# Performance work log

Hardware: AMD Instinct MI355X
Metric: run time of the kernel (lower is better)

Reference implementation:

```python
import jax, jax.numpy as jnp
import numpy as np
from jax import lax

DN = ('NCHW', 'OIHW', 'NCHW')


def conv3x3(x, w, groups=1):
    return lax.conv_general_dilated(x, w, window_strides=(1, 1),
                                    padding=((1, 1), (1, 1)),
                                    dimension_numbers=DN,
                                    feature_group_count=groups)


def conv1x1(x, w):
    return lax.conv_general_dilated(x, w, window_strides=(1, 1),
                                    padding=((0, 0), (0, 0)),
                                    dimension_numbers=DN)


def l2_normalize(t, eps=1e-12):
    n = jnp.sqrt(jnp.sum(t * t, axis=-1, keepdims=True))
    return t / jnp.maximum(n, eps)


def setup_inputs() -> dict:
    key = jax.random.key(0)
    ks = jax.random.split(key, 10)
    B, C, H, W = 4, 64, 256, 256
    heads = 8
    s = 0.05
    return {
        'x': jax.random.normal(ks[0], (B, C, H, W), jnp.float32),
        'w_iem': jax.random.normal(ks[1], (C, C, 3, 3), jnp.float32) * s,
        'w_nem': jax.random.normal(ks[2], (C, C, 3, 3), jnp.float32) * s,
        'w_iem_dw': jax.random.normal(ks[3], (C, 1, 3, 3), jnp.float32) * s,
        'w_nem_dw': jax.random.normal(ks[4], (C, 1, 3, 3), jnp.float32) * s,
        'w_q': jax.random.normal(ks[5], (C, C, 1, 1), jnp.float32) * s,
        'w_k': jax.random.normal(ks[6], (C, C, 1, 1), jnp.float32) * s,
        'w_v': jax.random.normal(ks[7], (C, C, 1, 1), jnp.float32) * s,
        'w_proj': jax.random.normal(ks[8], (C, C, 1, 1), jnp.float32) * s,
        'temperature': jnp.ones((1, heads, 1, 1, 1, 1), jnp.float32),
    }


def igam_forward(x, w_iem, w_nem, w_iem_dw, w_nem_dw, w_q, w_k, w_v, w_proj,
                 temperature, num_heads=8, window_size=8):
    b, c, h, w = x.shape
    ws = window_size
    pad_h = (ws - h % ws) % ws
    pad_w = (ws - w % ws) % ws
    if pad_h or pad_w:  # replicate pad on right/bottom (static)
        x = jnp.pad(x, ((0, 0), (0, 0), (0, pad_h), (0, pad_w)), mode='edge')
    hp, wp = x.shape[-2:]
    heads = num_heads
    d = c // heads
    nh, nw = hp // ws, wp // ws

    illumination_map = conv3x3(jax.nn.sigmoid(conv3x3(x, w_iem)), w_iem_dw, groups=c)
    noise_map = conv3x3(jax.nn.sigmoid(conv3x3(x, w_nem)), w_nem_dw, groups=c)
    illum_scalar = jnp.mean(illumination_map, axis=1, keepdims=True)  # (b,1,hp,wp)
    noise_scalar = jnp.mean(noise_map, axis=1, keepdims=True)

    q = conv1x1(illumination_map, w_q)
    k = conv1x1(noise_map, w_k)
    v = conv1x1(x, w_v)

    def to_windows(t):  # (b,c,hp,wp) -> (b,heads,nh,nw,ws*ws,d)
        t = t.reshape(b, heads, d, hp, wp).transpose(0, 1, 3, 4, 2)
        t = t.reshape(b, heads, nh, ws, nw, ws, d).transpose(0, 1, 2, 4, 3, 5, 6)
        return t.reshape(b, heads, nh, nw, ws * ws, d)

    def scalar_to_windows(t):  # (b,1,hp,wp) -> (b,1,nh,nw,ws*ws,1)
        t = t.reshape(b, 1, nh, ws, nw, ws).transpose(0, 1, 2, 4, 3, 5)
        return t.reshape(b, 1, nh, nw, ws * ws, 1)

    qw = l2_normalize(to_windows(q)) * (1.0 + scalar_to_windows(illum_scalar))
    kw = l2_normalize(to_windows(k)) * jnp.clip(1.0 - scalar_to_windows(noise_scalar), 0.0, 1.0)
    vw = to_windows(v)

    scale = d ** (-0.5)
    attn = jnp.einsum('bhnmqd,bhnmkd->bhnmqk', qw, kw) * scale * temperature
    attn = jax.nn.softmax(attn, axis=-1)
    outw = jnp.einsum('bhnmqk,bhnmkd->bhnmqd', attn, vw)

    # merge windows back to (b, c, hp, wp)
    outw = outw.reshape(b, heads, nh, nw, ws, ws, d).transpose(0, 1, 6, 2, 4, 3, 5)
    out = outw.reshape(b, heads * d, nh * ws, nw * ws)
    if pad_h or pad_w:
        out = out[:, :, :h, :w]
    return conv1x1(out, w_proj)


def reference(x, w_iem, w_nem, w_iem_dw, w_nem_dw, w_q, w_k, w_v, w_proj,
              temperature):
    return igam_forward(x, w_iem, w_nem, w_iem_dw, w_nem_dw, w_q, w_k, w_v,
                        w_proj, temperature)
```

## Files before the change

### kernel.cpp

```cpp
#include <hip/hip_runtime.h>
#include <math.h>

#define W_ 256
#define H_ 256
#define HW 65536
#define CC 64

typedef _Float16 h16;
typedef _Float16 half8 __attribute__((ext_vector_type(8)));
typedef float f32x4  __attribute__((ext_vector_type(4)));
typedef float f32x16 __attribute__((ext_vector_type(16)));

__device__ __forceinline__ unsigned pk2(float a, float b) {
  union { h16 h[2]; unsigned u; } c;
  c.h[0] = (h16)a; c.h[1] = (h16)b;
  return c.u;
}
__device__ __forceinline__ void plswap(unsigned &a, unsigned &b) {
  asm volatile("v_permlane32_swap_b32 %0, %1" : "+v"(a), "+v"(b));
}

__global__ __launch_bounds__(256) void k_wprep(
    const float* __restrict__ wi, const float* __restrict__ wn, h16* __restrict__ Bt)
{
  int i = blockIdx.x * 256 + threadIdx.x;
  if (i >= 128 * 576) return;
  int co = i / 576, k = i - co * 576;
  int tap = k >> 6, ci = k & 63;
  const float* src = (co < 64) ? wi : wn;
  int c = co & 63;
  Bt[i] = (h16)src[(c * 64 + ci) * 9 + tap];
}

__global__ __launch_bounds__(256) void k_wprep2(
    const float* __restrict__ wq, const float* __restrict__ wk,
    const float* __restrict__ wv, const float* __restrict__ wp,
    const float* __restrict__ wdw1, const float* __restrict__ wdw2,
    h16* __restrict__ W)
{
  int i = blockIdx.x * 256 + threadIdx.x;
  if (i >= 17536) return;
  if (i < 16384) {
    int m = i >> 12, e = i & 4095;
    const float* s = (m == 0) ? wq : (m == 1) ? wk : (m == 2) ? wv : wp;
    W[i] = (h16)s[e];
  } else {
    int e = i - 16384;
    int pass = e / 576, rem = e - pass * 576;
    int tap = rem >> 6, c = rem & 63;
    const float* s = pass ? wdw2 : wdw1;
    W[i] = (h16)s[c * 9 + tap];
  }
}

__global__ __launch_bounds__(256) void k_xpose(
    const float* __restrict__ x, h16* __restrict__ xT)
{
  __shared__ __align__(16) char sm[64 * 132];
  const int tid = threadIdx.x;
  const int xt = blockIdx.x, y = blockIdx.y, b = blockIdx.z;
  const int x0 = xt * 64;
  const float* xb = x + ((size_t)b * CC) * HW + y * W_ + x0;
  const int ci = tid >> 2, q = tid & 3;
#pragma unroll
  for (int k = 0; k < 4; ++k) {
    const int pc = q + k * 4;
    float4 v = *(const float4*)(xb + (size_t)ci * HW + pc * 4);
    const int px = pc * 4;
    *(h16*)(sm + (px + 0) * 132 + ci * 2) = (h16)v.x;
    *(h16*)(sm + (px + 1) * 132 + ci * 2) = (h16)v.y;
    *(h16*)(sm + (px + 2) * 132 + ci * 2) = (h16)v.z;
    *(h16*)(sm + (px + 3) * 132 + ci * 2) = (h16)v.w;
  }
  __syncthreads();
  h16* dst = xT + (((size_t)b * 256 + y) * 256 + x0) * 64;
#pragma unroll
  for (int it = 0; it < 2; ++it) {
    int task = tid + it * 256;
    int px = task >> 3, c8 = task & 7;
    int4 d = *(const int4*)(sm + px * 132 + c8 * 16);
    *(int4*)(dst + px * 64 + c8 * 8) = d;
  }
}

__global__ __launch_bounds__(512) void k_conv3x3x2(
    const h16* __restrict__ xT, const h16* __restrict__ Bt,
    h16* __restrict__ T1, h16* __restrict__ T2)
{
  __shared__ __align__(16) char lds[38016];

  const int tid = threadIdx.x;
  const int b = blockIdx.z, ry = blockIdx.y, cx = blockIdx.x;
  const int y0 = ry * 2, x0 = cx * 64;

  {
    const h16* xb = xT + ((size_t)b * 256) * 256 * 64;
    int4 zero4; zero4.x = zero4.y = zero4.z = zero4.w = 0;
#pragma unroll
    for (int it = 0; it < 5; ++it) {
      int idx = tid + it * 512;
      if (idx < 2112) {
        int pxr = idx >> 3, c8 = idx & 7;
        int r = pxr / 66, c = pxr - r * 66;
        int gy = y0 - 1 + r, gx = x0 - 1 + c;
        int4 d = zero4;
        if ((unsigned)gy < 256u && (unsigned)gx < 256u)
          d = *(const int4*)(xb + ((size_t)(gy * 256 + gx)) * 64 + c8 * 8);
        *(int4*)(lds + pxr * 144 + c8 * 16) = d;
      }
    }
  }
  __syncthreads();

  const int wv = tid >> 6, lane = tid & 63;
  const int wn_ = wv & 3;
  const int wm_ = wv >> 2;
  const int cob = wn_ * 32;
  const int pxb = wm_ * 64;
  const int lg = lane >> 4, lr = lane & 15;

  const char* pB[4];
#pragma unroll
  for (int pi = 0; pi < 4; ++pi) {
    int opx = (pxb + pi * 16 + lr) & 63;
    pB[pi] = lds + (wm_ * 66 + opx) * 144 + lg * 16;
  }
  const h16* wb0 = Bt + (size_t)(cob + lr) * 576 + lg * 8;
  const h16* wb1 = wb0 + 16 * 576;

  f32x4 acc[2][4];
#pragma unroll
  for (int i = 0; i < 2; ++i)
#pragma unroll
    for (int j = 0; j < 4; ++j) acc[i][j] = (f32x4){0.f, 0.f, 0.f, 0.f};

#pragma unroll
  for (int tap = 0; tap < 9; ++tap) {
    const int dy = tap / 3, dx = tap - dy * 3;
#pragma unroll
    for (int kh = 0; kh < 2; ++kh) {
      const int loff = (dy * 66 + dx) * 144 + kh * 64;
      const int koff = tap * 64 + kh * 32;
      half8 a0 = *(const half8*)(wb0 + koff);
      half8 a1 = *(const half8*)(wb1 + koff);
      half8 b0 = *(const half8*)(pB[0] + loff);
      half8 b1 = *(const half8*)(pB[1] + loff);
      half8 b2 = *(const half8*)(pB[2] + loff);
      half8 b3 = *(const half8*)(pB[3] + loff);
      acc[0][0] = __builtin_amdgcn_mfma_f32_16x16x32_f16(a0, b0, acc[0][0], 0, 0, 0);
      acc[0][1] = __builtin_amdgcn_mfma_f32_16x16x32_f16(a0, b1, acc[0][1], 0, 0, 0);
      acc[0][2] = __builtin_amdgcn_mfma_f32_16x16x32_f16(a0, b2, acc[0][2], 0, 0, 0);
      acc[0][3] = __builtin_amdgcn_mfma_f32_16x16x32_f16(a0, b3, acc[0][3], 0, 0, 0);
      acc[1][0] = __builtin_amdgcn_mfma_f32_16x16x32_f16(a1, b0, acc[1][0], 0, 0, 0);
      acc[1][1] = __builtin_amdgcn_mfma_f32_16x16x32_f16(a1, b1, acc[1][1], 0, 0, 0);
      acc[1][2] = __builtin_amdgcn_mfma_f32_16x16x32_f16(a1, b2, acc[1][2], 0, 0, 0);
      acc[1][3] = __builtin_amdgcn_mfma_f32_16x16x32_f16(a1, b3, acc[1][3], 0, 0, 0);
    }
  }
  __syncthreads();

#pragma unroll
  for (int ni = 0; ni < 2; ++ni) {
#pragma unroll
    for (int pi = 0; pi < 4; ++pi) {
      const int opx = (pxb + pi * 16 + lr) & 63;
      const int pxid = wm_ * 64 + opx;
      const int co = cob + ni * 16 + lg * 4;
      float s0 = 1.f / (1.f + __expf(-acc[ni][pi][0]));
      float s1 = 1.f / (1.f + __expf(-acc[ni][pi][1]));
      float s2 = 1.f / (1.f + __expf(-acc[ni][pi][2]));
      float s3 = 1.f / (1.f + __expf(-acc[ni][pi][3]));
      uint2 d; d.x = pk2(s0, s1); d.y = pk2(s2, s3);
      *(uint2*)(lds + pxid * 272 + co * 2) = d;
    }
  }
  __syncthreads();

  {
    int px = tid >> 3, chg = tid & 7;
#pragma unroll
    for (int seg = 0; seg < 4; ++seg) {
      int t = seg >> 1, rr = seg & 1;
      int4 d = *(const int4*)(lds + (rr * 64 + px) * 272 + t * 128 + chg * 16);
      h16* dst = (t ? T2 : T1) + (((size_t)b * 256 + (y0 + rr)) * 256 + (x0 + px)) * 64 + chg * 8;
      *(int4*)dst = d;
    }
  }
}

#define HALO 0
#define DWW  14400
#define SIN  16704
#define INA  17216
#define INB  26432
#define INC  35648

__global__ __launch_bounds__(256, 3) void k_megaattn(
    const h16* __restrict__ T1g, const h16* __restrict__ T2g,
    const h16* __restrict__ xT, const h16* __restrict__ Wall,
    const float* __restrict__ temp, float* __restrict__ out)
{
  __shared__ __align__(16) char sm[44864];
  const int tid = threadIdx.x;
  const int wv = tid >> 6, lane = tid & 63;
  const int lg = lane >> 4, lr = lane & 15;

  const int u = blockIdx.x;
  const int xcd = u & 7, idx = u >> 3;
  const int flat = xcd * 512 + idx;
  const int b = flat >> 10, rem = flat & 1023;
  const int wy = rem >> 5, wx = rem & 31;
  const int y0 = wy * 8, x0 = wx * 8;

  half8 wf[4][2];
#pragma unroll
  for (int m = 0; m < 4; ++m)
#pragma unroll
    for (int ks = 0; ks < 2; ++ks)
      wf[m][ks] = *(const half8*)(Wall + m * 4096 + (wv * 16 + lr) * 64 + ks * 32 + lg * 8);
  const float t0 = temp[wv * 2], t1 = temp[wv * 2 + 1];

  int4 zero4; zero4.x = zero4.y = zero4.z = zero4.w = 0;
  int4 h1r[4], h2r[4], xtr[2];
#pragma unroll
  for (int i = 0; i < 4; ++i) {
    int cc = tid + i * 256;
    bool act = cc < 800;
    int prow = act ? (cc >> 3) : 0;
    int c8 = cc & 7;
    int hy = prow / 10, hx = prow - hy * 10;
    int gy = y0 - 1 + hy, gx = x0 - 1 + hx;
    bool ok = act && (unsigned)gy < 256u && (unsigned)gx < 256u;
    size_t ga = (((size_t)b * 256 + gy) * 256 + gx) * (size_t)64 + c8 * 8;
    h1r[i] = ok ? *(const int4*)(T1g + ga) : zero4;
    h2r[i] = ok ? *(const int4*)(T2g + ga) : zero4;
  }
  const size_t wbase = (((size_t)b * 256 + y0) * 256 + x0) * 64;
#pragma unroll
  for (int it = 0; it < 2; ++it) {
    int p = tid + it * 256;
    int py = p >> 6, off = p & 63;
    xtr[it] = *(const int4*)(xT + wbase + (size_t)py * 16384 + off * 8);
  }

#pragma unroll
  for (int i = 0; i < 4; ++i) {
    int cc = tid + i * 256;
    if (cc < 800) *(int4*)(sm + HALO + (cc >> 3) * 144 + (cc & 7) * 16) = h1r[i];
  }
#pragma unroll
  for (int it = 0; it < 2; ++it) {
    int p = tid + it * 256;
    int py = p >> 6, off = p & 63;
    int px = py * 8 + (off >> 3);
    *(int4*)(sm + INC + px * 144 + (off & 7) * 16) = xtr[it];
  }
  if (tid < 144) {
    int4 d = *(const int4*)(Wall + 16384 + tid * 8);
    *(int4*)(sm + DWW + tid * 16) = d;
  }
  __syncthreads();

#pragma unroll
  for (int pass = 0; pass < 2; ++pass) {
    const int outb = pass ? INB : INA;
#pragma unroll
    for (int it = 0; it < 2; ++it) {
      const int task = it * 256 + tid;
      const int px = task >> 3, c8 = task & 7;
      const int py = px >> 3, pxx = px & 7;
      float a[8];
#pragma unroll
      for (int j = 0; j < 8; ++j) a[j] = 0.f;
#pragma unroll
      for (int tap = 0; tap < 9; ++tap) {
        const int dy = tap / 3, dx = tap - dy * 3;
        half8 v  = *(const half8*)(sm + HALO + ((py + dy) * 10 + pxx + dx) * 144 + c8 * 16);
        half8 w8 = *(const half8*)(sm + DWW + pass * 1152 + tap * 128 + c8 * 16);
#pragma unroll
        for (int j = 0; j < 8; ++j) a[j] = fmaf((float)v[j], (float)w8[j], a[j]);
      }
      half8 o;
#pragma unroll
      for (int j = 0; j < 8; ++j) o[j] = (h16)a[j];
      *(half8*)(sm + outb + px * 144 + c8 * 16) = o;
    }
    __syncthreads();
    if (pass == 0) {
#pragma unroll
      for (int i = 0; i < 4; ++i) {
        int cc = tid + i * 256;
        if (cc < 800) *(int4*)(sm + HALO + (cc >> 3) * 144 + (cc & 7) * 16) = h2r[i];
      }
      __syncthreads();
    }
  }

  if (tid < 128) {
    int which = tid >> 6, px = tid & 63;
    const char* row = sm + (which ? INB : INA) + px * 144;
    float s = 0.f;
#pragma unroll
    for (int j = 0; j < 8; ++j) {
      half8 v = *(const half8*)(row + j * 16);
#pragma unroll
      for (int e = 0; e < 8; ++e) s += (float)v[e];
    }
    *(float*)(sm + SIN + which * 256 + px * 4) = s * (1.f / 64.f);
  }
  __syncthreads();

  f32x4 aq[4], ak[4], av[4];
#pragma unroll
  for (int pi = 0; pi < 4; ++pi) {
    aq[pi] = (f32x4){0.f, 0.f, 0.f, 0.f};
    ak[pi] = (f32x4){0.f, 0.f, 0.f, 0.f};
    av[pi] = (f32x4){0.f, 0.f, 0.f, 0.f};
  }
#pragma unroll
  for (int pi = 0; pi < 4; ++pi)
#pragma unroll
    for (int ks = 0; ks < 2; ++ks) {
      const int boff = (pi * 16 + lr) * 144 + ks * 64 + lg * 16;
      half8 b0 = *(const half8*)(sm + INA + boff);
      half8 b1 = *(const half8*)(sm + INB + boff);
      half8 b2 = *(const half8*)(sm + INC + boff);
      aq[pi] = __builtin_amdgcn_mfma_f32_16x16x32_f16(wf[0][ks], b0, aq[pi], 0, 0, 0);
      ak[pi] = __builtin_amdgcn_mfma_f32_16x16x32_f16(wf[1][ks], b1, ak[pi], 0, 0, 0);
      av[pi] = __builtin_amdgcn_mfma_f32_16x16x32_f16(wf[2][ks], b2, av[pi], 0, 0, 0);
    }
  __syncthreads();

  const float th = (lg & 2) ? t1 : t0;
#pragma unroll
  for (int pi = 0; pi < 4; ++pi) {
    const int px = pi * 16 + lr;
    const float si = *(const float*)(sm + SIN + px * 4);
    const float sn = *(const float*)(sm + SIN + 256 + px * 4);
    float s2 = aq[pi][0]*aq[pi][0] + aq[pi][1]*aq[pi][1] + aq[pi][2]*aq[pi][2] + aq[pi][3]*aq[pi][3];
    float qs = (1.f + si) * 0.35355339059327373f * th /
               fmaxf(sqrtf(s2 + __shfl_xor(s2, 16)), 1e-12f);
    float k2 = ak[pi][0]*ak[pi][0] + ak[pi][1]*ak[pi][1] + ak[pi][2]*ak[pi][2] + ak[pi][3]*ak[pi][3];
    float ks2 = fminf(fmaxf(1.f - sn, 0.f), 1.f) /
                fmaxf(sqrtf(k2 + __shfl_xor(k2, 16)), 1e-12f);
    uint2 dq; dq.x = pk2(aq[pi][0]*qs, aq[pi][1]*qs); dq.y = pk2(aq[pi][2]*qs, aq[pi][3]*qs);
    uint2 dk; dk.x = pk2(ak[pi][0]*ks2, ak[pi][1]*ks2); dk.y = pk2(ak[pi][2]*ks2, ak[pi][3]*ks2);
    *(uint2*)(sm + INA + px * 144 + (wv * 16 + lg * 4) * 2) = dq;
    *(uint2*)(sm + INB + px * 144 + (wv * 16 + lg * 4) * 2) = dk;
#pragma unroll
    for (int r = 0; r < 4; ++r)
      *(h16*)(sm + INC + (wv * 16 + lg * 4 + r) * 144 + px * 2) = (h16)av[pi][r];
  }
  __syncthreads();

  const int l31 = lane & 31, hi = lane >> 5;
  const half8 hz = {(h16)0, (h16)0, (h16)0, (h16)0, (h16)0, (h16)0, (h16)0, (h16)0};
  const f32x16 z16 = {0.f,0.f,0.f,0.f,0.f,0.f,0.f,0.f,0.f,0.f,0.f,0.f,0.f,0.f,0.f,0.f};

#pragma unroll
  for (int t = 0; t < 2; ++t) {
    const int h = wv * 2 + t;
    half8 kfr[2], qfr[2];
#pragma unroll
    for (int kt = 0; kt < 2; ++kt)
      kfr[kt] = hi ? hz : *(const half8*)(sm + INB + (kt * 32 + l31) * 144 + h * 16);
#pragma unroll
    for (int qt = 0; qt < 2; ++qt)
      qfr[qt] = hi ? hz : *(const half8*)(sm + INA + (qt * 32 + l31) * 144 + h * 16);

#pragma unroll
    for (int qt = 0; qt < 2; ++qt) {
      f32x16 s0 = __builtin_amdgcn_mfma_f32_32x32x16_f16(kfr[0], qfr[qt], z16, 0, 0, 0);
      f32x16 s1 = __builtin_amdgcn_mfma_f32_32x32x16_f16(kfr[1], qfr[qt], z16, 0, 0, 0);
      float mx = s0[0];
#pragma unroll
      for (int i = 1; i < 16; ++i) mx = fmaxf(mx, s0[i]);
#pragma unroll
      for (int i = 0; i < 16; ++i) mx = fmaxf(mx, s1[i]);
      mx = fmaxf(mx, __shfl_xor(mx, 32));
      float sum = 0.f;
#pragma unroll
      for (int i = 0; i < 16; ++i) { s0[i] = __expf(s0[i] - mx); sum += s0[i]; }
#pragma unroll
      for (int i = 0; i < 16; ++i) { s1[i] = __expf(s1[i] - mx); sum += s1[i]; }
      sum += __shfl_xor(sum, 32);
      const float inv = 1.f / sum;
#pragma unroll
      for (int i = 0; i < 16; ++i) { s0[i] *= inv; s1[i] *= inv; }

      half8 pa[4];
#pragma unroll
      for (int st = 0; st < 4; ++st) {
        const int rb = (st & 1) * 8;
        float p0, p1, p2, p3, p4, p5, p6, p7;
        if (st < 2) {
          p0 = s0[rb+0]; p1 = s0[rb+1]; p2 = s0[rb+2]; p3 = s0[rb+3];
          p4 = s0[rb+4]; p5 = s0[rb+5]; p6 = s0[rb+6]; p7 = s0[rb+7];
        } else {
          p0 = s1[rb+0]; p1 = s1[rb+1]; p2 = s1[rb+2]; p3 = s1[rb+3];
          p4 = s1[rb+4]; p5 = s1[rb+5]; p6 = s1[rb+6]; p7 = s1[rb+7];
        }
        unsigned x0_ = pk2(p0, p1), x1_ = pk2(p2, p3);
        unsigned y0_ = pk2(p4, p5), y1_ = pk2(p6, p7);
        plswap(x0_, y0_);
        plswap(x1_, y1_);
        union { unsigned uu4[4]; half8 h; } uu;
        uu.uu4[0] = x0_; uu.uu4[1] = x1_; uu.uu4[2] = y0_; uu.uu4[3] = y1_;
        pa[st] = uu.h;
      }
      f32x16 oacc = z16;
#pragma unroll
      for (int st = 0; st < 4; ++st) {
        half8 vfr = (l31 < 8)
          ? *(const half8*)(sm + INC + (h * 8 + l31) * 144 + (st * 16 + hi * 8) * 2)
          : hz;
        oacc = __builtin_amdgcn_mfma_f32_32x32x16_f16(pa[st], vfr, oacc, 0, 0, 0);
      }
      if (l31 < 8) {
#pragma unroll
        for (int r = 0; r < 16; ++r) {
          const int q = qt * 32 + (r & 3) + 8 * (r >> 2) + 4 * hi;
          *(h16*)(sm + INA + q * 144 + (h * 8 + l31) * 2) = (h16)oacc[r];
        }
      }
    }
  }
  __syncthreads();

  f32x4 pacc[4];
#pragma unroll
  for (int pi = 0; pi < 4; ++pi) pacc[pi] = (f32x4){0.f, 0.f, 0.f, 0.f};
#pragma unroll
  for (int pi = 0; pi < 4; ++pi)
#pragma unroll
    for (int ks = 0; ks < 2; ++ks) {
      half8 bfr = *(const half8*)(sm + INA + (pi * 16 + lr) * 144 + ks * 64 + lg * 16);
      pacc[pi] = __builtin_amdgcn_mfma_f32_16x16x32_f16(wf[3][ks], bfr, pacc[pi], 0, 0, 0);
    }
#pragma unroll
  for (int pi = 0; pi < 4; ++pi) {
    const int px = pi * 16 + lr;
    const int py = px >> 3, pxx = px & 7;
    const int co = wv * 16 + lg * 4;
    float* ob = out + ((size_t)(b * CC + co)) * HW + (size_t)(y0 + py) * W_ + (x0 + pxx);
    ob[0]      = pacc[pi][0];
    ob[HW]     = pacc[pi][1];
    ob[2 * HW] = pacc[pi][2];
    ob[3 * HW] = pacc[pi][3];
  }
}

extern "C" void kernel_launch(void* const* d_in, const int* in_sizes, int n_in,
                              void* d_out, int out_size, void* d_ws, size_t ws_size,
                              hipStream_t stream) {
  const float* x        = (const float*)d_in[0];
  const float* w_iem    = (const float*)d_in[1];
  const float* w_nem    = (const float*)d_in[2];
  const float* w_iem_dw = (const float*)d_in[3];
  const float* w_nem_dw = (const float*)d_in[4];
  const float* w_q      = (const float*)d_in[5];
  const float* w_k      = (const float*)d_in[6];
  const float* w_v      = (const float*)d_in[7];
  const float* w_proj   = (const float*)d_in[8];
  const float* temp     = (const float*)d_in[9];
  float* outp = (float*)d_out;

  const size_t PLE = (size_t)4 * CC * HW;
  h16* h0   = (h16*)d_ws;
  h16* T1   = h0;
  h16* T2   = h0 + PLE;
  h16* xT   = h0 + 2 * PLE;
  h16* Bt   = h0 + 3 * PLE;
  h16* Wall = Bt + 73728;

  dim3 b256(256), b512(512);

  k_wprep    <<<dim3(288),        b256, 0, stream>>>(w_iem, w_nem, Bt);
  k_wprep2   <<<dim3(69),         b256, 0, stream>>>(w_q, w_k, w_v, w_proj,
                                                     w_iem_dw, w_nem_dw, Wall);
  k_xpose    <<<dim3(4, 256, 4),  b256, 0, stream>>>(x, xT);
  k_conv3x3x2<<<dim3(4, 128, 4),  b512, 0, stream>>>(xT, Bt, T1, T2);
  k_megaattn <<<dim3(4096),       b256, 0, stream>>>(T1, T2, xT, Wall, temp, outp);
}
```

Baseline: 228.0 us.

## Double megaattn block to 512 threads and compute depthwise conv in packed fp16

Launches the fused attention kernel with 512 threads per window instead of 256. Each wave now handles one head and half the pixels of the 1x1 projections, so per-thread loop trip counts halve and latency hiding can improve. The depthwise 3x3 now accumulates in fp16 packed vectors instead of fp32 FMAs, which cuts ALU work but loses accumulation precision. The launch-bounds request of 6 blocks of 512 threads per CU may squeeze registers and force spills.

```diff
diff --git a/kernel.cpp b/kernel.cpp
--- a/kernel.cpp
+++ b/kernel.cpp
@@ -195,7 +195,7 @@
 #define INB  26432
 #define INC  35648
 
-__global__ __launch_bounds__(256, 3) void k_megaattn(
+__global__ __launch_bounds__(512, 6) void k_megaattn(
     const h16* __restrict__ T1g, const h16* __restrict__ T2g,
     const h16* __restrict__ xT, const h16* __restrict__ Wall,
     const float* __restrict__ temp, float* __restrict__ out)
@@ -204,6 +204,8 @@
   const int tid = threadIdx.x;
   const int wv = tid >> 6, lane = tid & 63;
   const int lg = lane >> 4, lr = lane & 15;
+  const int wn = wv & 3;
+  const int wm = wv >> 2;
 
   const int u = blockIdx.x;
   const int xcd = u & 7, idx = u >> 3;
@@ -217,14 +219,14 @@
   for (int m = 0; m < 4; ++m)
 #pragma unroll
     for (int ks = 0; ks < 2; ++ks)
-      wf[m][ks] = *(const half8*)(Wall + m * 4096 + (wv * 16 + lr) * 64 + ks * 32 + lg * 8);
-  const float t0 = temp[wv * 2], t1 = temp[wv * 2 + 1];
+      wf[m][ks] = *(const half8*)(Wall + m * 4096 + (wn * 16 + lr) * 64 + ks * 32 + lg * 8);
+  const float thv = temp[wn * 2 + (lg >> 1)];
 
   int4 zero4; zero4.x = zero4.y = zero4.z = zero4.w = 0;
-  int4 h1r[4], h2r[4], xtr[2];
-#pragma unroll
-  for (int i = 0; i < 4; ++i) {
-    int cc = tid + i * 256;
+  int4 h1r[2], h2r[2], xtr;
+#pragma unroll
+  for (int i = 0; i < 2; ++i) {
+    int cc = tid + i * 512;
     bool act = cc < 800;
     int prow = act ? (cc >> 3) : 0;
     int c8 = cc & 7;
@@ -236,24 +238,17 @@
     h2r[i] = ok ? *(const int4*)(T2g + ga) : zero4;
   }
   const size_t wbase = (((size_t)b * 256 + y0) * 256 + x0) * 64;
-#pragma unroll
-  for (int it = 0; it < 2; ++it) {
-    int p = tid + it * 256;
-    int py = p >> 6, off = p & 63;
-    xtr[it] = *(const int4*)(xT + wbase + (size_t)py * 16384 + off * 8);
-  }
-
-#pragma unroll
-  for (int i = 0; i < 4; ++i) {
-    int cc = tid + i * 256;
+  xtr = *(const int4*)(xT + wbase + (size_t)(tid >> 6) * 16384 + (tid & 63) * 8);
+
+#pragma unroll
+  for (int i = 0; i < 2; ++i) {
+    int cc = tid + i * 512;
     if (cc < 800) *(int4*)(sm + HALO + (cc >> 3) * 144 + (cc & 7) * 16) = h1r[i];
   }
-#pragma unroll
-  for (int it = 0; it < 2; ++it) {
-    int p = tid + it * 256;
-    int py = p >> 6, off = p & 63;
+  {
+    int py = tid >> 6, off = tid & 63;
     int px = py * 8 + (off >> 3);
-    *(int4*)(sm + INC + px * 144 + (off & 7) * 16) = xtr[it];
+    *(int4*)(sm + INC + px * 144 + (off & 7) * 16) = xtr;
   }
   if (tid < 144) {
     int4 d = *(const int4*)(Wall + 16384 + tid * 8);
@@ -261,35 +256,28 @@
   }
   __syncthreads();
 
+  const half8 hz8 = {(h16)0, (h16)0, (h16)0, (h16)0, (h16)0, (h16)0, (h16)0, (h16)0};
 #pragma unroll
   for (int pass = 0; pass < 2; ++pass) {
     const int outb = pass ? INB : INA;
-#pragma unroll
-    for (int it = 0; it < 2; ++it) {
-      const int task = it * 256 + tid;
-      const int px = task >> 3, c8 = task & 7;
+    {
+      const int px = tid >> 3, c8 = tid & 7;
       const int py = px >> 3, pxx = px & 7;
-      float a[8];
-#pragma unroll
-      for (int j = 0; j < 8; ++j) a[j] = 0.f;
+      half8 af = hz8;
 #pragma unroll
       for (int tap = 0; tap < 9; ++tap) {
         const int dy = tap / 3, dx = tap - dy * 3;
         half8 v  = *(const half8*)(sm + HALO + ((py + dy) * 10 + pxx + dx) * 144 + c8 * 16);
         half8 w8 = *(const half8*)(sm + DWW + pass * 1152 + tap * 128 + c8 * 16);
-#pragma unroll
-        for (int j = 0; j < 8; ++j) a[j] = fmaf((float)v[j], (float)w8[j], a[j]);
-      }
-      half8 o;
-#pragma unroll
-      for (int j = 0; j < 8; ++j) o[j] = (h16)a[j];
-      *(half8*)(sm + outb + px * 144 + c8 * 16) = o;
+        af += v * w8;
+      }
+      *(half8*)(sm + outb + px * 144 + c8 * 16) = af;
     }
     __syncthreads();
     if (pass == 0) {
 #pragma unroll
-      for (int i = 0; i < 4; ++i) {
-        int cc = tid + i * 256;
+      for (int i = 0; i < 2; ++i) {
+        int cc = tid + i * 512;
         if (cc < 800) *(int4*)(sm + HALO + (cc >> 3) * 144 + (cc & 7) * 16) = h2r[i];
       }
       __syncthreads();
@@ -310,18 +298,18 @@
   }
   __syncthreads();
 
-  f32x4 aq[4], ak[4], av[4];
-#pragma unroll
-  for (int pi = 0; pi < 4; ++pi) {
+  f32x4 aq[2], ak[2], av[2];
+#pragma unroll
+  for (int pi = 0; pi < 2; ++pi) {
     aq[pi] = (f32x4){0.f, 0.f, 0.f, 0.f};
     ak[pi] = (f32x4){0.f, 0.f, 0.f, 0.f};
     av[pi] = (f32x4){0.f, 0.f, 0.f, 0.f};
   }
 #pragma unroll
-  for (int pi = 0; pi < 4; ++pi)
+  for (int pi = 0; pi < 2; ++pi)
 #pragma unroll
     for (int ks = 0; ks < 2; ++ks) {
-      const int boff = (pi * 16 + lr) * 144 + ks * 64 + lg * 16;
+      const int boff = (wm * 32 + pi * 16 + lr) * 144 + ks * 64 + lg * 16;
       half8 b0 = *(const half8*)(sm + INA + boff);
       half8 b1 = *(const half8*)(sm + INB + boff);
       half8 b2 = *(const half8*)(sm + INC + boff);
@@ -331,35 +319,32 @@
     }
   __syncthreads();
 
-  const float th = (lg & 2) ? t1 : t0;
-#pragma unroll
-  for (int pi = 0; pi < 4; ++pi) {
-    const int px = pi * 16 + lr;
+#pragma unroll
+  for (int pi = 0; pi < 2; ++pi) {
+    const int px = wm * 32 + pi * 16 + lr;
     const float si = *(const float*)(sm + SIN + px * 4);
     const float sn = *(const float*)(sm + SIN + 256 + px * 4);
     float s2 = aq[pi][0]*aq[pi][0] + aq[pi][1]*aq[pi][1] + aq[pi][2]*aq[pi][2] + aq[pi][3]*aq[pi][3];
-    float qs = (1.f + si) * 0.35355339059327373f * th /
+    float qs = (1.f + si) * 0.35355339059327373f * thv /
                fmaxf(sqrtf(s2 + __shfl_xor(s2, 16)), 1e-12f);
     float k2 = ak[pi][0]*ak[pi][0] + ak[pi][1]*ak[pi][1] + ak[pi][2]*ak[pi][2] + ak[pi][3]*ak[pi][3];
     float ks2 = fminf(fmaxf(1.f - sn, 0.f), 1.f) /
                 fmaxf(sqrtf(k2 + __shfl_xor(k2, 16)), 1e-12f);
     uint2 dq; dq.x = pk2(aq[pi][0]*qs, aq[pi][1]*qs); dq.y = pk2(aq[pi][2]*qs, aq[pi][3]*qs);
     uint2 dk; dk.x = pk2(ak[pi][0]*ks2, ak[pi][1]*ks2); dk.y = pk2(ak[pi][2]*ks2, ak[pi][3]*ks2);
-    *(uint2*)(sm + INA + px * 144 + (wv * 16 + lg * 4) * 2) = dq;
-    *(uint2*)(sm + INB + px * 144 + (wv * 16 + lg * 4) * 2) = dk;
+    *(uint2*)(sm + INA + px * 144 + (wn * 16 + lg * 4) * 2) = dq;
+    *(uint2*)(sm + INB + px * 144 + (wn * 16 + lg * 4) * 2) = dk;
 #pragma unroll
     for (int r = 0; r < 4; ++r)
-      *(h16*)(sm + INC + (wv * 16 + lg * 4 + r) * 144 + px * 2) = (h16)av[pi][r];
+      *(h16*)(sm + INC + (wn * 16 + lg * 4 + r) * 144 + px * 2) = (h16)av[pi][r];
   }
   __syncthreads();
 
   const int l31 = lane & 31, hi = lane >> 5;
-  const half8 hz = {(h16)0, (h16)0, (h16)0, (h16)0, (h16)0, (h16)0, (h16)0, (h16)0};
+  const half8 hz = hz8;
   const f32x16 z16 = {0.f,0.f,0.f,0.f,0.f,0.f,0.f,0.f,0.f,0.f,0.f,0.f,0.f,0.f,0.f,0.f};
-
-#pragma unroll
-  for (int t = 0; t < 2; ++t) {
-    const int h = wv * 2 + t;
+  {
+    const int h = wv;
     half8 kfr[2], qfr[2];
 #pragma unroll
     for (int kt = 0; kt < 2; ++kt)
@@ -427,21 +412,21 @@
   }
   __syncthreads();
 
-  f32x4 pacc[4];
-#pragma unroll
-  for (int pi = 0; pi < 4; ++pi) pacc[pi] = (f32x4){0.f, 0.f, 0.f, 0.f};
-#pragma unroll
-  for (int pi = 0; pi < 4; ++pi)
+  f32x4 pacc[2];
+#pragma unroll
+  for (int pi = 0; pi < 2; ++pi) pacc[pi] = (f32x4){0.f, 0.f, 0.f, 0.f};
+#pragma unroll
+  for (int pi = 0; pi < 2; ++pi)
 #pragma unroll
     for (int ks = 0; ks < 2; ++ks) {
-      half8 bfr = *(const half8*)(sm + INA + (pi * 16 + lr) * 144 + ks * 64 + lg * 16);
+      half8 bfr = *(const half8*)(sm + INA + (wm * 32 + pi * 16 + lr) * 144 + ks * 64 + lg * 16);
       pacc[pi] = __builtin_amdgcn_mfma_f32_16x16x32_f16(wf[3][ks], bfr, pacc[pi], 0, 0, 0);
     }
 #pragma unroll
-  for (int pi = 0; pi < 4; ++pi) {
-    const int px = pi * 16 + lr;
+  for (int pi = 0; pi < 2; ++pi) {
+    const int px = wm * 32 + pi * 16 + lr;
     const int py = px >> 3, pxx = px & 7;
-    const int co = wv * 16 + lg * 4;
+    const int co = wn * 16 + lg * 4;
     float* ob = out + ((size_t)(b * CC + co)) * HW + (size_t)(y0 + py) * W_ + (x0 + pxx);
     ob[0]      = pacc[pi][0];
     ob[HW]     = pacc[pi][1];
@@ -480,5 +465,5 @@
                                                      w_iem_dw, w_nem_dw, Wall);
   k_xpose    <<<dim3(4, 256, 4),  b256, 0, stream>>>(x, xT);
   k_conv3x3x2<<<dim3(4, 128, 4),  b512, 0, stream>>>(xT, Bt, T1, T2);
-  k_megaattn <<<dim3(4096),       b256, 0, stream>>>(T1, T2, xT, Wall, temp, outp);
-}
+  k_megaattn <<<dim3(4096),       b512, 0, stream>>>(T1, T2, xT, Wall, temp, outp);
+}
```

New measurement: 204.2 us. 1.12x faster.
